# Performance work log

Hardware: AMD Instinct MI355X
Metric: run time of the kernel (lower is better)

The kernel has to match this reference:

```python
import jax, jax.numpy as jnp
import numpy as np

DECAY = 0.8
EPS = 1e-05
COMMIT_W = 0.25
N, D, K = 32768, 128, 4096


def setup_inputs() -> dict:
    key = jax.random.key(0)
    k1, k2, k3, k4 = jax.random.split(key, 4)
    x = jax.random.normal(k1, (N, D), dtype=jnp.float32)
    embed = jax.random.normal(k2, (1, K, D), dtype=jnp.float32)
    cluster_size = jax.random.uniform(k3, (1, K), dtype=jnp.float32)
    embed_avg = jax.random.normal(k4, (1, K, D), dtype=jnp.float32)
    return {"x": x, "embed": embed, "cluster_size": cluster_size, "embed_avg": embed_avg}


def reference(x, embed, cluster_size, embed_avg):
    # x: [n, d]; embed: [1, K, d] (num_codebooks = 1, squeezed as in batched_embedding)
    e = embed[0]                                   # [K, d]
    K_ = e.shape[0]
    # negative squared euclidean distance (== -cdist^2 ordering, same argmin as -cdist)
    x2 = jnp.sum(x * x, axis=-1, keepdims=True)    # [n, 1]
    e2 = jnp.sum(e * e, axis=-1)                   # [K]
    dist = -(x2 - 2.0 * (x @ e.T) + e2)            # [n, K]
    embed_ind = jnp.argmax(dist, axis=-1)          # [n] cluster assignment (argmin distance)
    # differentiable embedding lookup (one-hot @ embed == gather)
    quantize = jnp.take(e, embed_ind, axis=0)      # [n, d]
    # EMA codebook statistics (training-time buffer updates)
    ones = jnp.ones((x.shape[0],), dtype=x.dtype)
    bins = jax.ops.segment_sum(ones, embed_ind, num_segments=K_)         # [K] bincount
    embed_sum = jax.ops.segment_sum(x, embed_ind, num_segments=K_)       # [K, d] scatter-add
    cs_new = cluster_size[0] * DECAY + (1.0 - DECAY) * bins
    ea_new = embed_avg[0] * DECAY + (1.0 - DECAY) * embed_sum
    n_total = jnp.sum(cs_new)
    cluster = (cs_new + EPS) / (n_total + K_ * EPS) * n_total            # laplace smoothing
    embed_normalized = ea_new / cluster[:, None]                         # [K, d]
    # commitment loss: mse(quantize.detach(), x) * weight
    commit_loss = COMMIT_W * jnp.mean((jax.lax.stop_gradient(quantize) - x) ** 2)
    return (quantize, embed_ind, commit_loss, cs_new[None], embed_normalized[None])
```

## Files before the change

kernel.cpp:

```cpp
#include <hip/hip_runtime.h>

#define NROWS 32768
#define DIM   128
#define KCODES 4096
#define DECAYF 0.8f
#define EPSF 1e-5f
#define COMMITW 0.25f

typedef _Float16 half8 __attribute__((ext_vector_type(8)));
typedef _Float16 half2v __attribute__((ext_vector_type(2)));
typedef float float4v __attribute__((ext_vector_type(4)));

__global__ __launch_bounds__(256) void esplit_kernel(const float* __restrict__ embed,
                                                     _Float16* __restrict__ estg,
                                                     float* __restrict__ e2h) {
    int code = blockIdx.x * 4 + (threadIdx.x >> 6);
    int lane = threadIdx.x & 63;
    float2 v = ((const float2*)(embed + (size_t)code * DIM))[lane];
    float s = v.x * v.x + v.y * v.y;
    #pragma unroll
    for (int off = 32; off > 0; off >>= 1) s += __shfl_down(s, off, 64);
    if (lane == 0) e2h[code] = 0.5f * s;

    int d = lane * 2;
    int ks = d >> 5, q = (d >> 3) & 3, j = d & 7;
    _Float16 h0 = (_Float16)v.x, l0 = (_Float16)(v.x - (float)h0);
    _Float16 h1 = (_Float16)v.y, l1 = (_Float16)(v.y - (float)h1);
    int chunk = code >> 6, c6 = code & 63;
    size_t base = (size_t)chunk * 16384;
    size_t hidx = base + (size_t)(( 0 + ks * 4 + q) * 64 + c6) * 8 + j;
    size_t lidx = base + (size_t)((16 + ks * 4 + q) * 64 + c6) * 8 + j;
    *(half2v*)&estg[hidx] = (half2v){h0, h1};
    *(half2v*)&estg[lidx] = (half2v){l0, l1};
}

__global__ __launch_bounds__(512, 2) void argmax_kernel(const float* __restrict__ x,
                                                        const _Float16* __restrict__ estg,
                                                        const float* __restrict__ e2h,
                                                        int* __restrict__ ind,
                                                        float* __restrict__ out_ind,
                                                        int* __restrict__ bins,
                                                        float* __restrict__ loss) {
    __shared__ float rv[8][64];
    __shared__ int   ri[8][64];
    __shared__ float x2s[128];

    int tid = threadIdx.x;
    int lane = tid & 63;
    int w = tid >> 6;
    int j = w & 3;
    int rh = w >> 2;
    int m15 = lane & 15;
    int q = (lane >> 4) & 3;
    int n0 = blockIdx.x * 128;

    half8 Ah[4][4], Al[4][4];
    float xsq[4];
    #pragma unroll
    for (int rt = 0; rt < 4; ++rt) {
        xsq[rt] = 0.f;
        #pragma unroll
        for (int ks = 0; ks < 4; ++ks) {
            const float* p = x + (size_t)(n0 + rh * 64 + rt * 16 + m15) * DIM + ks * 32 + q * 8;
            float4 a = *(const float4*)p;
            float4 b = *(const float4*)(p + 4);
            float f[8] = {a.x, a.y, a.z, a.w, b.x, b.y, b.z, b.w};
            half8 H, L;
            #pragma unroll
            for (int e = 0; e < 8; ++e) {
                _Float16 h = (_Float16)f[e];
                H[e] = h;
                L[e] = (_Float16)(f[e] - (float)h);
                xsq[rt] += f[e] * f[e];
            }
            Ah[rt][ks] = H;
            Al[rt][ks] = L;
        }
        xsq[rt] += __shfl_xor(xsq[rt], 16, 64);
        xsq[rt] += __shfl_xor(xsq[rt], 32, 64);
    }
    if (j == 0 && lane < 16) {
        #pragma unroll
        for (int rt = 0; rt < 4; ++rt) x2s[rh * 64 + rt * 16 + m15] = xsq[rt];
    }

    float best[4][4];
    int   bidx[4][4];
    #pragma unroll
    for (int rt = 0; rt < 4; ++rt)
        #pragma unroll
        for (int r = 0; r < 4; ++r) { best[rt][r] = -3.0e38f; bidx[rt][r] = 0; }

    const _Float16* bbase = estg + (size_t)(j * 16 + m15) * 8 + (size_t)q * 512;
    const int cm = j * 16 + m15;

    half8 B0h[4], B0l[4], B1h[4], B1l[4];
    float e20, e21;

    {
        const _Float16* cb = bbase;
        #pragma unroll
        for (int ks = 0; ks < 4; ++ks) {
            B0h[ks] = *(const half8*)(cb + ks * 2048);
            B0l[ks] = *(const half8*)(cb + 8192 + ks * 2048);
        }
        e20 = e2h[cm];
    }

    #pragma unroll 1
    for (int ch = 0; ch < 64; ch += 2) {
        {
            const _Float16* cb = bbase + (size_t)(ch + 1) * 16384;
            #pragma unroll
            for (int ks = 0; ks < 4; ++ks) {
                B1h[ks] = *(const half8*)(cb + ks * 2048);
                B1l[ks] = *(const half8*)(cb + 8192 + ks * 2048);
            }
            e21 = e2h[(ch + 1) * 64 + cm];
        }
        {
            float4v acc[4];
            #pragma unroll
            for (int rt = 0; rt < 4; ++rt) acc[rt] = (float4v){-e20, -e20, -e20, -e20};
            #pragma unroll
            for (int ks = 0; ks < 4; ++ks)
                #pragma unroll
                for (int rt = 0; rt < 4; ++rt) {
                    acc[rt] = __builtin_amdgcn_mfma_f32_16x16x32_f16(Ah[rt][ks], B0h[ks], acc[rt], 0, 0, 0);
                    acc[rt] = __builtin_amdgcn_mfma_f32_16x16x32_f16(Al[rt][ks], B0h[ks], acc[rt], 0, 0, 0);
                    acc[rt] = __builtin_amdgcn_mfma_f32_16x16x32_f16(Ah[rt][ks], B0l[ks], acc[rt], 0, 0, 0);
                }
            int c = ch * 64 + cm;
            #pragma unroll
            for (int rt = 0; rt < 4; ++rt)
                #pragma unroll
                for (int r = 0; r < 4; ++r) {
                    float s = acc[rt][r];
                    if (s > best[rt][r]) { best[rt][r] = s; bidx[rt][r] = c; }
                }
        }
        if (ch + 2 < 64) {
            const _Float16* cb = bbase + (size_t)(ch + 2) * 16384;
            #pragma unroll
            for (int ks = 0; ks < 4; ++ks) {
                B0h[ks] = *(const half8*)(cb + ks * 2048);
                B0l[ks] = *(const half8*)(cb + 8192 + ks * 2048);
            }
            e20 = e2h[(ch + 2) * 64 + cm];
        }
        {
            float4v acc[4];
            #pragma unroll
            for (int rt = 0; rt < 4; ++rt) acc[rt] = (float4v){-e21, -e21, -e21, -e21};
            #pragma unroll
            for (int ks = 0; ks < 4; ++ks)
                #pragma unroll
                for (int rt = 0; rt < 4; ++rt) {
                    acc[rt] = __builtin_amdgcn_mfma_f32_16x16x32_f16(Ah[rt][ks], B1h[ks], acc[rt], 0, 0, 0);
                    acc[rt] = __builtin_amdgcn_mfma_f32_16x16x32_f16(Al[rt][ks], B1h[ks], acc[rt], 0, 0, 0);
                    acc[rt] = __builtin_amdgcn_mfma_f32_16x16x32_f16(Ah[rt][ks], B1l[ks], acc[rt], 0, 0, 0);
                }
            int c = (ch + 1) * 64 + cm;
            #pragma unroll
            for (int rt = 0; rt < 4; ++rt)
                #pragma unroll
                for (int r = 0; r < 4; ++r) {
                    float s = acc[rt][r];
                    if (s > best[rt][r]) { best[rt][r] = s; bidx[rt][r] = c; }
                }
        }
    }

    #pragma unroll
    for (int rt = 0; rt < 4; ++rt)
        #pragma unroll
        for (int r = 0; r < 4; ++r) {
            float bv = best[rt][r];
            int   bi = bidx[rt][r];
            #pragma unroll
            for (int m = 1; m <= 8; m <<= 1) {
                float ov = __shfl_xor(bv, m, 64);
                int   oi = __shfl_xor(bi, m, 64);
                if (ov > bv || (ov == bv && oi < bi)) { bv = ov; bi = oi; }
            }
            if (m15 == 0) {
                int rl = rt * 16 + q * 4 + r;
                rv[w][rl] = bv;
                ri[w][rl] = bi;
            }
        }
    __syncthreads();
    if (tid < 128) {
        int rhh = tid >> 6;
        int rl  = tid & 63;
        float bv = rv[rhh * 4][rl];
        int   bi = ri[rhh * 4][rl];
        #pragma unroll
        for (int jj = 1; jj < 4; ++jj) {
            float ov = rv[rhh * 4 + jj][rl];
            int   oi = ri[rhh * 4 + jj][rl];
            if (ov > bv || (ov == bv && oi < bi)) { bv = ov; bi = oi; }
        }
        ind[n0 + tid] = bi;
        out_ind[n0 + tid] = (float)bi;
        atomicAdd(&bins[bi], 1);
        float lp = x2s[tid] - 2.0f * bv;
        #pragma unroll
        for (int off = 32; off > 0; off >>= 1) lp += __shfl_down(lp, off, 64);
        if ((tid & 63) == 0) atomicAdd(loss, lp);
    }
}

__global__ __launch_bounds__(1024) void scan_kernel(const int* __restrict__ bins,
                                                    const float* __restrict__ cluster_size,
                                                    const float* __restrict__ loss,
                                                    int* __restrict__ offsets,
                                                    int* __restrict__ cursor,
                                                    float* __restrict__ out_cs,
                                                    float* __restrict__ ntot,
                                                    float* __restrict__ out_loss) {
    __shared__ int   wtot[16];
    __shared__ float fred[16];
    int t = threadIdx.x;
    int lane = t & 63, wv = t >> 6;
    int b[4];
    float cs[4];
    float csum = 0.f;
    int s = 0;
    #pragma unroll
    for (int e = 0; e < 4; ++e) {
        b[e] = bins[t * 4 + e];
        s += b[e];
        cs[e] = cluster_size[t * 4 + e] * DECAYF + (1.0f - DECAYF) * (float)b[e];
        csum += cs[e];
    }
    int sc = s;
    #pragma unroll
    for (int off = 1; off < 64; off <<= 1) {
        int v = __shfl_up(sc, off, 64);
        if (lane >= off) sc += v;
    }
    float fc = csum;
    #pragma unroll
    for (int off = 32; off > 0; off >>= 1) fc += __shfl_down(fc, off, 64);
    if (lane == 63) wtot[wv] = sc;
    if (lane == 0) fred[wv] = fc;
    __syncthreads();
    if (t < 16) {
        int v = wtot[t];
        int scv = v;
        #pragma unroll
        for (int off = 1; off < 16; off <<= 1) {
            int u = __shfl_up(scv, off, 64);
            if (t >= off) scv += u;
        }
        wtot[t] = scv - v;
    }
    if (t == 0) {
        float tot = 0.f;
        #pragma unroll
        for (int i = 0; i < 16; ++i) tot += fred[i];
        *ntot = tot;
        *out_loss = COMMITW * (*loss) / (float)((size_t)NROWS * DIM);
    }
    __syncthreads();
    int ex = sc - s + wtot[wv];
    #pragma unroll
    for (int e = 0; e < 4; ++e) {
        offsets[t * 4 + e] = ex;
        cursor[t * 4 + e] = ex;
        out_cs[t * 4 + e] = cs[e];
        ex += b[e];
    }
}

__global__ __launch_bounds__(256) void reorder_kernel(const int* __restrict__ ind,
                                                      int* __restrict__ cursor,
                                                      int* __restrict__ rowids,
                                                      int* __restrict__ codesorted) {
    int row = blockIdx.x * 256 + threadIdx.x;
    int k = ind[row];
    int pos = atomicAdd(&cursor[k], 1);
    rowids[pos] = row;
    codesorted[pos] = k;
}

#define WROWS 16
__global__ __launch_bounds__(256) void segred_kernel(const float* __restrict__ x,
                                                     const float* __restrict__ embed,
                                                     const int* __restrict__ rowids,
                                                     const int* __restrict__ codesorted,
                                                     const int* __restrict__ offsets,
                                                     const int* __restrict__ bins,
                                                     float* __restrict__ esum,
                                                     float* __restrict__ out_q) {
    int tid = threadIdx.x;
    int lane = tid & 63;
    int wv = blockIdx.x * 4 + (tid >> 6);
    int w0 = wv * WROWS;

    int i16 = lane & (WROWS - 1);
    int rowv = rowids[w0 + i16];
    int kv   = codesorted[w0 + i16];

    float2 xv[WROWS];
    #pragma unroll
    for (int i = 0; i < WROWS; ++i) {
        int row = __shfl(rowv, i, 64);
        xv[i] = ((const float2*)(x + (size_t)row * DIM))[lane];
    }

    int curk = __shfl(kv, 0, 64);
    float2 qv = ((const float2*)(embed + (size_t)curk * DIM))[lane];
    float2 acc = {0.f, 0.f};

    #pragma unroll
    for (int i = 0; i < WROWS; ++i) {
        int row = __shfl(rowv, i, 64);
        int k   = __shfl(kv, i, 64);
        if (k != curk) {
            int sbeg = offsets[curk];
            int send = sbeg + bins[curk];
            float* ep = esum + (size_t)curk * DIM + lane * 2;
            if (sbeg >= w0 && send <= w0 + WROWS) {
                *(float2*)ep = acc;
            } else {
                atomicAdd(ep, acc.x);
                atomicAdd(ep + 1, acc.y);
            }
            curk = k;
            acc = (float2){0.f, 0.f};
            qv = ((const float2*)(embed + (size_t)curk * DIM))[lane];
        }
        acc.x += xv[i].x;
        acc.y += xv[i].y;
        ((float2*)(out_q + (size_t)row * DIM))[lane] = qv;
    }
    {
        int sbeg = offsets[curk];
        int send = sbeg + bins[curk];
        float* ep = esum + (size_t)curk * DIM + lane * 2;
        if (sbeg >= w0 && send <= w0 + WROWS) {
            *(float2*)ep = acc;
        } else {
            atomicAdd(ep, acc.x);
            atomicAdd(ep + 1, acc.y);
        }
    }
}

__global__ __launch_bounds__(256) void norm_kernel(const float* __restrict__ esum,
                                                   const float* __restrict__ embed_avg,
                                                   const float* __restrict__ out_cs,
                                                   const float* __restrict__ ntot,
                                                   float* __restrict__ out_norm) {
    int idx = blockIdx.x * 256 + threadIdx.x;
    int k = idx >> 6;
    float nt = *ntot;
    float cs = out_cs[k];
    float cluster = (cs + EPSF) / (nt + (float)KCODES * EPSF) * nt;
    float inv = 1.0f / cluster;
    float2 es = ((const float2*)esum)[idx];
    float2 ea = ((const float2*)embed_avg)[idx];
    float2 o;
    o.x = (ea.x * DECAYF + (1.0f - DECAYF) * es.x) * inv;
    o.y = (ea.y * DECAYF + (1.0f - DECAYF) * es.y) * inv;
    ((float2*)out_norm)[idx] = o;
}

extern "C" void kernel_launch(void* const* d_in, const int* in_sizes, int n_in,
                              void* d_out, int out_size, void* d_ws, size_t ws_size,
                              hipStream_t stream) {
    const float* x            = (const float*)d_in[0];
    const float* embed        = (const float*)d_in[1];
    const float* cluster_size = (const float*)d_in[2];
    const float* embed_avg    = (const float*)d_in[3];

    float* out      = (float*)d_out;
    float* out_q    = out;
    float* out_ind  = out + 4194304;
    float* out_loss = out_ind + 32768;
    float* out_cs   = out_loss + 1;
    float* out_norm = out_cs + 4096;

    char* ws = (char*)d_ws;
    _Float16* estg = (_Float16*)ws;
    float* e2h   = (float*)(ws + 2097152);
    int*   ind   = (int*)(ws + 2113536);
    int*   offsets = (int*)(ws + 2244608);
    int*   cursor  = (int*)(ws + 2260992);
    int*   rowids  = (int*)(ws + 2277376);
    int*   codesorted = (int*)(ws + 2408448);
    float* loss  = (float*)(ws + 2539520);
    float* ntot  = loss + 1;
    int*   bins  = (int*)(ws + 2539776);
    float* esum  = (float*)(ws + 2556160);

    hipMemsetAsync(ws + 2539520, 0, 256 + 16384 + 2097152, stream);

    esplit_kernel<<<KCODES / 4, 256, 0, stream>>>(embed, estg, e2h);
    argmax_kernel<<<NROWS / 128, 512, 0, stream>>>(x, estg, e2h, ind, out_ind,
                                                   bins, loss);
    scan_kernel<<<1, 1024, 0, stream>>>(bins, cluster_size, loss, offsets, cursor,
                                        out_cs, ntot, out_loss);
    reorder_kernel<<<NROWS / 256, 256, 0, stream>>>(ind, cursor, rowids, codesorted);
    segred_kernel<<<NROWS / WROWS / 4, 256, 0, stream>>>(x, embed, rowids, codesorted,
                                                         offsets, bins, esum, out_q);
    norm_kernel<<<KCODES * DIM / 2 / 256, 256, 0, stream>>>(esum, embed_avg, out_cs,
                                                            ntot, out_norm);
}
```

Baseline: 193.1 us.

## Switch argmax to 32x32 MFMA tiles and fuse normalization into segment reduce

The argmax GEMM moves from 16x16x32 to 32x32x16 MFMA. Each wave now owns a 32-row by 32-code tile, and the staged codebook layout is changed to match. The separate norm kernel is removed. Codes with no assigned rows are normalized inside the scan kernel, and all other codes are normalized in segred, either directly or by the last contributor, detected with a per-code done counter plus threadfence. This drops a launch and a full pass over esum. The cost is a serial per-thread loop over empty codes in the single-block scan kernel and extra atomics and fences on split segments.

Result: slower. 390.8 us (+102.3%).

```diff
diff --git a/kernel.cpp b/kernel.cpp
--- a/kernel.cpp
+++ b/kernel.cpp
@@ -9,7 +9,7 @@
 
 typedef _Float16 half8 __attribute__((ext_vector_type(8)));
 typedef _Float16 half2v __attribute__((ext_vector_type(2)));
-typedef float float4v __attribute__((ext_vector_type(4)));
+typedef float float16v __attribute__((ext_vector_type(16)));
 
 __global__ __launch_bounds__(256) void esplit_kernel(const float* __restrict__ embed,
                                                      _Float16* __restrict__ estg,
@@ -23,13 +23,13 @@
     if (lane == 0) e2h[code] = 0.5f * s;
 
     int d = lane * 2;
-    int ks = d >> 5, q = (d >> 3) & 3, j = d & 7;
+    int ks = d >> 4, kh = (d >> 3) & 1, j = d & 7;
     _Float16 h0 = (_Float16)v.x, l0 = (_Float16)(v.x - (float)h0);
     _Float16 h1 = (_Float16)v.y, l1 = (_Float16)(v.y - (float)h1);
     int chunk = code >> 6, c6 = code & 63;
     size_t base = (size_t)chunk * 16384;
-    size_t hidx = base + (size_t)(( 0 + ks * 4 + q) * 64 + c6) * 8 + j;
-    size_t lidx = base + (size_t)((16 + ks * 4 + q) * 64 + c6) * 8 + j;
+    size_t hidx = base + (size_t)(( 0 + ks * 2 + kh) * 64 + c6) * 8 + j;
+    size_t lidx = base + (size_t)((16 + ks * 2 + kh) * 64 + c6) * 8 + j;
     *(half2v*)&estg[hidx] = (half2v){h0, h1};
     *(half2v*)&estg[lidx] = (half2v){l0, l1};
 }
@@ -41,29 +41,27 @@
                                                         float* __restrict__ out_ind,
                                                         int* __restrict__ bins,
                                                         float* __restrict__ loss) {
-    __shared__ float rv[8][64];
-    __shared__ int   ri[8][64];
+    __shared__ float rv[2][128];
+    __shared__ int   ri[2][128];
     __shared__ float x2s[128];
 
     int tid = threadIdx.x;
     int lane = tid & 63;
     int w = tid >> 6;
-    int j = w & 3;
-    int rh = w >> 2;
-    int m15 = lane & 15;
-    int q = (lane >> 4) & 3;
+    int ct = w & 1;
+    int rt = w >> 1;
+    int n31 = lane & 31;
+    int kh = lane >> 5;
     int n0 = blockIdx.x * 128;
 
-    half8 Ah[4][4], Al[4][4];
-    float xsq[4];
-    #pragma unroll
-    for (int rt = 0; rt < 4; ++rt) {
-        xsq[rt] = 0.f;
-        #pragma unroll
-        for (int ks = 0; ks < 4; ++ks) {
-            const float* p = x + (size_t)(n0 + rh * 64 + rt * 16 + m15) * DIM + ks * 32 + q * 8;
-            float4 a = *(const float4*)p;
-            float4 b = *(const float4*)(p + 4);
+    half8 Ah[8], Al[8];
+    float xsq = 0.f;
+    {
+        const float* xr = x + (size_t)(n0 + rt * 32 + n31) * DIM + kh * 8;
+        #pragma unroll
+        for (int ks = 0; ks < 8; ++ks) {
+            float4 a = *(const float4*)(xr + ks * 16);
+            float4 b = *(const float4*)(xr + ks * 16 + 4);
             float f[8] = {a.x, a.y, a.z, a.w, b.x, b.y, b.z, b.w};
             half8 H, L;
             #pragma unroll
@@ -71,38 +69,32 @@
                 _Float16 h = (_Float16)f[e];
                 H[e] = h;
                 L[e] = (_Float16)(f[e] - (float)h);
-                xsq[rt] += f[e] * f[e];
-            }
-            Ah[rt][ks] = H;
-            Al[rt][ks] = L;
-        }
-        xsq[rt] += __shfl_xor(xsq[rt], 16, 64);
-        xsq[rt] += __shfl_xor(xsq[rt], 32, 64);
-    }
-    if (j == 0 && lane < 16) {
-        #pragma unroll
-        for (int rt = 0; rt < 4; ++rt) x2s[rh * 64 + rt * 16 + m15] = xsq[rt];
-    }
-
-    float best[4][4];
-    int   bidx[4][4];
-    #pragma unroll
-    for (int rt = 0; rt < 4; ++rt)
-        #pragma unroll
-        for (int r = 0; r < 4; ++r) { best[rt][r] = -3.0e38f; bidx[rt][r] = 0; }
-
-    const _Float16* bbase = estg + (size_t)(j * 16 + m15) * 8 + (size_t)q * 512;
-    const int cm = j * 16 + m15;
-
-    half8 B0h[4], B0l[4], B1h[4], B1l[4];
+                xsq += f[e] * f[e];
+            }
+            Ah[ks] = H;
+            Al[ks] = L;
+        }
+        xsq += __shfl_xor(xsq, 32, 64);
+        if (ct == 0 && kh == 0) x2s[rt * 32 + n31] = xsq;
+    }
+
+    float best[16];
+    int   bidx[16];
+    #pragma unroll
+    for (int r = 0; r < 16; ++r) { best[r] = -3.0e38f; bidx[r] = 0; }
+
+    const _Float16* bbase = estg + (size_t)(kh * 64 + ct * 32 + n31) * 8;
+    const int cm = ct * 32 + n31;
+
+    half8 B0h[8], B0l[8], B1h[8], B1l[8];
     float e20, e21;
 
     {
         const _Float16* cb = bbase;
         #pragma unroll
-        for (int ks = 0; ks < 4; ++ks) {
-            B0h[ks] = *(const half8*)(cb + ks * 2048);
-            B0l[ks] = *(const half8*)(cb + 8192 + ks * 2048);
+        for (int ks = 0; ks < 8; ++ks) {
+            B0h[ks] = *(const half8*)(cb + (size_t)ks * 1024);
+            B0l[ks] = *(const half8*)(cb + 8192 + (size_t)ks * 1024);
         }
         e20 = e2h[cm];
     }
@@ -112,95 +104,76 @@
         {
             const _Float16* cb = bbase + (size_t)(ch + 1) * 16384;
             #pragma unroll
-            for (int ks = 0; ks < 4; ++ks) {
-                B1h[ks] = *(const half8*)(cb + ks * 2048);
-                B1l[ks] = *(const half8*)(cb + 8192 + ks * 2048);
+            for (int ks = 0; ks < 8; ++ks) {
+                B1h[ks] = *(const half8*)(cb + (size_t)ks * 1024);
+                B1l[ks] = *(const half8*)(cb + 8192 + (size_t)ks * 1024);
             }
             e21 = e2h[(ch + 1) * 64 + cm];
         }
         {
-            float4v acc[4];
-            #pragma unroll
-            for (int rt = 0; rt < 4; ++rt) acc[rt] = (float4v){-e20, -e20, -e20, -e20};
-            #pragma unroll
-            for (int ks = 0; ks < 4; ++ks)
-                #pragma unroll
-                for (int rt = 0; rt < 4; ++rt) {
-                    acc[rt] = __builtin_amdgcn_mfma_f32_16x16x32_f16(Ah[rt][ks], B0h[ks], acc[rt], 0, 0, 0);
-                    acc[rt] = __builtin_amdgcn_mfma_f32_16x16x32_f16(Al[rt][ks], B0h[ks], acc[rt], 0, 0, 0);
-                    acc[rt] = __builtin_amdgcn_mfma_f32_16x16x32_f16(Ah[rt][ks], B0l[ks], acc[rt], 0, 0, 0);
-                }
+            float16v acc;
+            #pragma unroll
+            for (int r = 0; r < 16; ++r) acc[r] = -e20;
+            #pragma unroll
+            for (int ks = 0; ks < 8; ++ks) {
+                acc = __builtin_amdgcn_mfma_f32_32x32x16_f16(Ah[ks], B0h[ks], acc, 0, 0, 0);
+                acc = __builtin_amdgcn_mfma_f32_32x32x16_f16(Al[ks], B0h[ks], acc, 0, 0, 0);
+                acc = __builtin_amdgcn_mfma_f32_32x32x16_f16(Ah[ks], B0l[ks], acc, 0, 0, 0);
+            }
             int c = ch * 64 + cm;
             #pragma unroll
-            for (int rt = 0; rt < 4; ++rt)
-                #pragma unroll
-                for (int r = 0; r < 4; ++r) {
-                    float s = acc[rt][r];
-                    if (s > best[rt][r]) { best[rt][r] = s; bidx[rt][r] = c; }
-                }
+            for (int r = 0; r < 16; ++r)
+                if (acc[r] > best[r]) { best[r] = acc[r]; bidx[r] = c; }
         }
         if (ch + 2 < 64) {
             const _Float16* cb = bbase + (size_t)(ch + 2) * 16384;
             #pragma unroll
-            for (int ks = 0; ks < 4; ++ks) {
-                B0h[ks] = *(const half8*)(cb + ks * 2048);
-                B0l[ks] = *(const half8*)(cb + 8192 + ks * 2048);
+            for (int ks = 0; ks < 8; ++ks) {
+                B0h[ks] = *(const half8*)(cb + (size_t)ks * 1024);
+                B0l[ks] = *(const half8*)(cb + 8192 + (size_t)ks * 1024);
             }
             e20 = e2h[(ch + 2) * 64 + cm];
         }
         {
-            float4v acc[4];
-            #pragma unroll
-            for (int rt = 0; rt < 4; ++rt) acc[rt] = (float4v){-e21, -e21, -e21, -e21};
-            #pragma unroll
-            for (int ks = 0; ks < 4; ++ks)
-                #pragma unroll
-                for (int rt = 0; rt < 4; ++rt) {
-                    acc[rt] = __builtin_amdgcn_mfma_f32_16x16x32_f16(Ah[rt][ks], B1h[ks], acc[rt], 0, 0, 0);
-                    acc[rt] = __builtin_amdgcn_mfma_f32_16x16x32_f16(Al[rt][ks], B1h[ks], acc[rt], 0, 0, 0);
-                    acc[rt] = __builtin_amdgcn_mfma_f32_16x16x32_f16(Ah[rt][ks], B1l[ks], acc[rt], 0, 0, 0);
-                }
+            float16v acc;
+            #pragma unroll
+            for (int r = 0; r < 16; ++r) acc[r] = -e21;
+            #pragma unroll
+            for (int ks = 0; ks < 8; ++ks) {
+                acc = __builtin_amdgcn_mfma_f32_32x32x16_f16(Ah[ks], B1h[ks], acc, 0, 0, 0);
+                acc = __builtin_amdgcn_mfma_f32_32x32x16_f16(Al[ks], B1h[ks], acc, 0, 0, 0);
+                acc = __builtin_amdgcn_mfma_f32_32x32x16_f16(Ah[ks], B1l[ks], acc, 0, 0, 0);
+            }
             int c = (ch + 1) * 64 + cm;
             #pragma unroll
-            for (int rt = 0; rt < 4; ++rt)
-                #pragma unroll
-                for (int r = 0; r < 4; ++r) {
-                    float s = acc[rt][r];
-                    if (s > best[rt][r]) { best[rt][r] = s; bidx[rt][r] = c; }
-                }
-        }
-    }
-
-    #pragma unroll
-    for (int rt = 0; rt < 4; ++rt)
-        #pragma unroll
-        for (int r = 0; r < 4; ++r) {
-            float bv = best[rt][r];
-            int   bi = bidx[rt][r];
-            #pragma unroll
-            for (int m = 1; m <= 8; m <<= 1) {
-                float ov = __shfl_xor(bv, m, 64);
-                int   oi = __shfl_xor(bi, m, 64);
-                if (ov > bv || (ov == bv && oi < bi)) { bv = ov; bi = oi; }
-            }
-            if (m15 == 0) {
-                int rl = rt * 16 + q * 4 + r;
-                rv[w][rl] = bv;
-                ri[w][rl] = bi;
-            }
-        }
+            for (int r = 0; r < 16; ++r)
+                if (acc[r] > best[r]) { best[r] = acc[r]; bidx[r] = c; }
+        }
+    }
+
+    #pragma unroll
+    for (int r = 0; r < 16; ++r) {
+        float bv = best[r];
+        int   bi = bidx[r];
+        #pragma unroll
+        for (int m = 1; m <= 16; m <<= 1) {
+            float ov = __shfl_xor(bv, m, 64);
+            int   oi = __shfl_xor(bi, m, 64);
+            if (ov > bv || (ov == bv && oi < bi)) { bv = ov; bi = oi; }
+        }
+        if (n31 == 0) {
+            int row = rt * 32 + (r & 3) + 8 * (r >> 2) + 4 * kh;
+            rv[ct][row] = bv;
+            ri[ct][row] = bi;
+        }
+    }
     __syncthreads();
     if (tid < 128) {
-        int rhh = tid >> 6;
-        int rl  = tid & 63;
-        float bv = rv[rhh * 4][rl];
-        int   bi = ri[rhh * 4][rl];
-        #pragma unroll
-        for (int jj = 1; jj < 4; ++jj) {
-            float ov = rv[rhh * 4 + jj][rl];
-            int   oi = ri[rhh * 4 + jj][rl];
-            if (ov > bv || (ov == bv && oi < bi)) { bv = ov; bi = oi; }
-        }
+        float bv = rv[0][tid];
+        int   bi = ri[0][tid];
+        float ov = rv[1][tid];
+        int   oi = ri[1][tid];
+        if (ov > bv || (ov == bv && oi < bi)) { bv = ov; bi = oi; }
         ind[n0 + tid] = bi;
         out_ind[n0 + tid] = (float)bi;
         atomicAdd(&bins[bi], 1);
@@ -214,13 +187,16 @@
 __global__ __launch_bounds__(1024) void scan_kernel(const int* __restrict__ bins,
                                                     const float* __restrict__ cluster_size,
                                                     const float* __restrict__ loss,
+                                                    const float* __restrict__ embed_avg,
                                                     int* __restrict__ offsets,
                                                     int* __restrict__ cursor,
                                                     float* __restrict__ out_cs,
                                                     float* __restrict__ ntot,
-                                                    float* __restrict__ out_loss) {
+                                                    float* __restrict__ out_loss,
+                                                    float* __restrict__ out_norm) {
     __shared__ int   wtot[16];
     __shared__ float fred[16];
+    __shared__ float stot;
     int t = threadIdx.x;
     int lane = t & 63, wv = t >> 6;
     int b[4];
@@ -260,17 +236,31 @@
         float tot = 0.f;
         #pragma unroll
         for (int i = 0; i < 16; ++i) tot += fred[i];
+        stot = tot;
         *ntot = tot;
         *out_loss = COMMITW * (*loss) / (float)((size_t)NROWS * DIM);
     }
     __syncthreads();
+    float nt = stot;
     int ex = sc - s + wtot[wv];
     #pragma unroll
     for (int e = 0; e < 4; ++e) {
-        offsets[t * 4 + e] = ex;
-        cursor[t * 4 + e] = ex;
-        out_cs[t * 4 + e] = cs[e];
+        int k = t * 4 + e;
+        offsets[k] = ex;
+        cursor[k] = ex;
+        out_cs[k] = cs[e];
         ex += b[e];
+        if (b[e] == 0) {
+            float cluster = (cs[e] + EPSF) / (nt + (float)KCODES * EPSF) * nt;
+            float coef = DECAYF / cluster;
+            float4* dst = (float4*)(out_norm + (size_t)k * DIM);
+            const float4* ea = (const float4*)(embed_avg + (size_t)k * DIM);
+            for (int i = 0; i < DIM / 4; ++i) {
+                float4 v = ea[i];
+                v.x *= coef; v.y *= coef; v.z *= coef; v.w *= coef;
+                dst[i] = v;
+            }
+        }
     }
 }
 
@@ -292,12 +282,18 @@
                                                      const int* __restrict__ codesorted,
                                                      const int* __restrict__ offsets,
                                                      const int* __restrict__ bins,
+                                                     const float* __restrict__ embed_avg,
+                                                     const float* __restrict__ out_cs,
+                                                     const float* __restrict__ ntot,
                                                      float* __restrict__ esum,
-                                                     float* __restrict__ out_q) {
+                                                     int* __restrict__ done,
+                                                     float* __restrict__ out_q,
+                                                     float* __restrict__ out_norm) {
     int tid = threadIdx.x;
     int lane = tid & 63;
     int wv = blockIdx.x * 4 + (tid >> 6);
     int w0 = wv * WROWS;
+    float nt = *ntot;
 
     int i16 = lane & (WROWS - 1);
     int rowv = rowids[w0 + i16];
@@ -311,24 +307,53 @@
     }
 
     int curk = __shfl(kv, 0, 64);
+    int runstart = 0;
     float2 qv = ((const float2*)(embed + (size_t)curk * DIM))[lane];
     float2 acc = {0.f, 0.f};
 
     #pragma unroll
-    for (int i = 0; i < WROWS; ++i) {
-        int row = __shfl(rowv, i, 64);
-        int k   = __shfl(kv, i, 64);
-        if (k != curk) {
+    for (int i = 0; i <= WROWS; ++i) {
+        int row = 0, k = 0;
+        if (i < WROWS) {
+            row = __shfl(rowv, i, 64);
+            k   = __shfl(kv, i, 64);
+        }
+        if (i == WROWS || k != curk) {
             int sbeg = offsets[curk];
-            int send = sbeg + bins[curk];
-            float* ep = esum + (size_t)curk * DIM + lane * 2;
-            if (sbeg >= w0 && send <= w0 + WROWS) {
-                *(float2*)ep = acc;
+            int cnt  = bins[curk];
+            float cs = out_cs[curk];
+            float cluster = (cs + EPSF) / (nt + (float)KCODES * EPSF) * nt;
+            float inv = 1.0f / cluster;
+            size_t idx = (size_t)curk * DIM + lane * 2;
+            if (sbeg >= w0 && sbeg + cnt <= w0 + WROWS) {
+                float2 ea = *(const float2*)(embed_avg + idx);
+                float2 o;
+                o.x = (ea.x * DECAYF + (1.0f - DECAYF) * acc.x) * inv;
+                o.y = (ea.y * DECAYF + (1.0f - DECAYF) * acc.y) * inv;
+                *(float2*)(out_norm + idx) = o;
             } else {
+                float* ep = esum + idx;
                 atomicAdd(ep, acc.x);
                 atomicAdd(ep + 1, acc.y);
-            }
+                __threadfence();
+                int rl = i - runstart;
+                int old = 0;
+                if (lane == 0) old = atomicAdd(&done[curk], rl);
+                old = __shfl(old, 0, 64);
+                if (old + rl == cnt) {
+                    __threadfence();
+                    float ex0 = atomicAdd(ep, 0.0f);
+                    float ex1 = atomicAdd(ep + 1, 0.0f);
+                    float2 ea = *(const float2*)(embed_avg + idx);
+                    float2 o;
+                    o.x = (ea.x * DECAYF + (1.0f - DECAYF) * ex0) * inv;
+                    o.y = (ea.y * DECAYF + (1.0f - DECAYF) * ex1) * inv;
+                    *(float2*)(out_norm + idx) = o;
+                }
+            }
+            if (i == WROWS) break;
             curk = k;
+            runstart = i;
             acc = (float2){0.f, 0.f};
             qv = ((const float2*)(embed + (size_t)curk * DIM))[lane];
         }
@@ -336,36 +361,6 @@
         acc.y += xv[i].y;
         ((float2*)(out_q + (size_t)row * DIM))[lane] = qv;
     }
-    {
-        int sbeg = offsets[curk];
-        int send = sbeg + bins[curk];
-        float* ep = esum + (size_t)curk * DIM + lane * 2;
-        if (sbeg >= w0 && send <= w0 + WROWS) {
-            *(float2*)ep = acc;
-        } else {
-            atomicAdd(ep, acc.x);
-            atomicAdd(ep + 1, acc.y);
-        }
-    }
-}
-
-__global__ __launch_bounds__(256) void norm_kernel(const float* __restrict__ esum,
-                                                   const float* __restrict__ embed_avg,
-                                                   const float* __restrict__ out_cs,
-                                                   const float* __restrict__ ntot,
-                                                   float* __restrict__ out_norm) {
-    int idx = blockIdx.x * 256 + threadIdx.x;
-    int k = idx >> 6;
-    float nt = *ntot;
-    float cs = out_cs[k];
-    float cluster = (cs + EPSF) / (nt + (float)KCODES * EPSF) * nt;
-    float inv = 1.0f / cluster;
-    float2 es = ((const float2*)esum)[idx];
-    float2 ea = ((const float2*)embed_avg)[idx];
-    float2 o;
-    o.x = (ea.x * DECAYF + (1.0f - DECAYF) * es.x) * inv;
-    o.y = (ea.y * DECAYF + (1.0f - DECAYF) * es.y) * inv;
-    ((float2*)out_norm)[idx] = o;
 }
 
 extern "C" void kernel_launch(void* const* d_in, const int* in_sizes, int n_in,
@@ -394,18 +389,20 @@
     float* loss  = (float*)(ws + 2539520);
     float* ntot  = loss + 1;
     int*   bins  = (int*)(ws + 2539776);
-    float* esum  = (float*)(ws + 2556160);
-
-    hipMemsetAsync(ws + 2539520, 0, 256 + 16384 + 2097152, stream);
+    int*   done  = (int*)(ws + 2556160);
+    float* esum  = (float*)(ws + 2572544);
+
+    hipMemsetAsync(ws + 2539520, 0, 256 + 16384 + 16384 + 2097152, stream);
 
     esplit_kernel<<<KCODES / 4, 256, 0, stream>>>(embed, estg, e2h);
     argmax_kernel<<<NROWS / 128, 512, 0, stream>>>(x, estg, e2h, ind, out_ind,
                                                    bins, loss);
-    scan_kernel<<<1, 1024, 0, stream>>>(bins, cluster_size, loss, offsets, cursor,
-                                        out_cs, ntot, out_loss);
+    scan_kernel<<<1, 1024, 0, stream>>>(bins, cluster_size, loss, embed_avg,
+                                        offsets, cursor, out_cs, ntot, out_loss,
+                                        out_norm);
     reorder_kernel<<<NROWS / 256, 256, 0, stream>>>(ind, cursor, rowids, codesorted);
     segred_kernel<<<NROWS / WROWS / 4, 256, 0, stream>>>(x, embed, rowids, codesorted,
-                                                         offsets, bins, esum, out_q);
-    norm_kernel<<<KCODES * DIM / 2 / 256, 256, 0, stream>>>(esum, embed_avg, out_cs,
-                                                            ntot, out_norm);
-}
+                                                         offsets, bins, embed_avg,
+                                                         out_cs, ntot, esum, done,
+                                                         out_q, out_norm);
+}
```
